# Kernel optimization log

Measured on AMD Instinct MI355X. Metric: run time of the kernel, lower is better.

The kernel has to match this reference:

```python
import jax, jax.numpy as jnp
import numpy as np

N_BITS = 32
HIDDEN = 128


def _neighborhoods(z):
    """z: (B,k,H,W) -> (B,k,9,H,W) 3x3 neighborhoods (zero-padded), center zeroed.

    Position ordering matches F.unfold(kernel_size=3): row-major over (di,dj),
    so index 4 is the center, which the module masks to 0.
    """
    B, k, H, W = z.shape
    zp = jnp.pad(z, ((0, 0), (0, 0), (1, 1), (1, 1)))
    views = []
    for di in range(3):
        for dj in range(3):
            if di == 1 and dj == 1:  # center masked out
                views.append(jnp.zeros_like(z))
            else:
                views.append(zp[:, :, di:di + H, dj:dj + W])
    return jnp.stack(views, axis=2)  # (B,k,9,H,W)


def setup_inputs() -> dict:
    key = jax.random.key(0)
    k1, k2, k3, k4, k5 = jax.random.split(key, 5)
    B, k, H, W = 8, N_BITS, 256, 256
    z = jax.random.normal(k1, (B, k, H, W), dtype=jnp.float32)
    # nn.Linear(9*k, hidden): weight (hidden, 9k), feature order = k-outer, 9-inner
    W1 = jax.random.normal(k2, (HIDDEN, 9 * k), dtype=jnp.float32) * (1.0 / np.sqrt(9 * k))
    b1 = jax.random.normal(k3, (HIDDEN,), dtype=jnp.float32) * 0.01
    W2 = jax.random.normal(k4, (k, HIDDEN), dtype=jnp.float32) * (1.0 / np.sqrt(HIDDEN))
    b2 = jax.random.normal(k5, (k,), dtype=jnp.float32) * 0.01
    return {"z": z, "W1": W1, "b1": b1, "W2": W2, "b2": b2}


def reference(z, W1, b1, W2, b2):
    B, k, H, W = z.shape
    win = _neighborhoods(z)                      # (B,k,9,H,W)
    W1r = W1.reshape(HIDDEN, k, 9)               # split (9k) -> (k,9), k-outer
    h = jnp.einsum('bkphw,dkp->bdhw', win, W1r) + b1[None, :, None, None]
    h = jax.nn.relu(h)
    logits = jnp.einsum('bdhw,kd->bkhw', h, W2) + b2[None, :, None, None]
    return logits  # (B,k,H,W)
```

## Files before the change

kernel.cpp:

```cpp
#include <hip/hip_runtime.h>


#define KC 32
#define HH 256
#define WW 256
#define HID 128
#define YS 8
#define ZROW 2640

typedef __attribute__((ext_vector_type(8))) short short8;
typedef __attribute__((ext_vector_type(4))) float f32x4;

#define BARRIER() asm volatile("s_waitcnt lgkmcnt(0)\n\ts_barrier" ::: "memory")
#define SCHED_FENCE() asm volatile("" ::: "memory")

__device__ __forceinline__ unsigned short f2bf(float f) {
    union { float f; unsigned int i; } x; x.f = f;
    unsigned int r = x.i + 0x7FFFu + ((x.i >> 16) & 1u);
    return (unsigned short)(r >> 16);
}

__device__ __forceinline__ short8 pack8(const float* v) {
    union { short8 s; unsigned int u[4]; } w;
    union { float f; unsigned int i; } uu[8];
#pragma unroll
    for (int j = 0; j < 8; ++j) uu[j].f = v[j];
#pragma unroll
    for (int k = 0; k < 4; ++k)
        w.u[k] = __builtin_amdgcn_perm(uu[2 * k + 1].i, uu[2 * k].i, 0x07060302u);
    return w.s;
}

__global__ void prep_weights(const float* __restrict__ w1,
                             const float* __restrict__ w2,
                             unsigned short* __restrict__ w1t,
                             unsigned short* __restrict__ w2t) {
    int i = blockIdx.x * 256 + threadIdx.x;
    if (i < 9 * HID * KC) {
        int c = i & 31;
        int d = (i >> 5) & 127;
        int p = i >> 12;
        w1t[i] = f2bf(w1[d * (9 * KC) + c * 9 + p]);
    } else if (i < 9 * HID * KC + KC * HID) {
        int j = i - 9 * HID * KC;
        w2t[j] = f2bf(w2[j]);
    }
}

__global__ __launch_bounds__(256, 3) void local_pred_kernel(
    const float* __restrict__ zg,
    const unsigned short* __restrict__ w1t,
    const float* __restrict__ b1g,
    const unsigned short* __restrict__ w2t,
    const float* __restrict__ b2g,
    float* __restrict__ outg)
{
    __shared__ __attribute__((aligned(16))) unsigned short z_lds[4 * ZROW];
    __shared__ __attribute__((aligned(16))) unsigned short h_lds[64 * 136];
    __shared__ __attribute__((aligned(16))) unsigned short halo_lds[7 * 2 * 32];

    const int tid  = threadIdx.x;
    const int bidx = blockIdx.x;
    const int x0 = (bidx & 3) << 6;
    const int y0 = ((bidx >> 2) & 31) * YS;
    const int b  = bidx >> 7;

    const int l = tid & 63;
    const int o = tid >> 6;

    const int wave = tid >> 6;
    const int lane = tid & 63;
    const int lr = lane & 15;
    const int lq = lane >> 4;

    const float* zb = zg + (size_t)b * KC * HH * WW;

#pragma unroll
    for (int dy = 0; dy < 3; ++dy) {
        const int gy = y0 - 1 + dy;
        const bool ok = (unsigned)gy < (unsigned)HH;
        const int gyc = ok ? gy : 0;
        const float* p = zb + ((size_t)(o * 8) * HH + gyc) * WW + x0 + l;
        float t8[8];
#pragma unroll
        for (int j = 0; j < 8; ++j) t8[j] = ok ? p[(size_t)j * HH * WW] : 0.f;
        *(short8*)&z_lds[(dy * 66 + l + 1) * 40 + o * 8] = pack8(t8);
        SCHED_FENCE();
    }
    {
        const int s = tid & 1, oc = (tid >> 1) & 3, dy = tid >> 3;
        const int gy = y0 - 1 + dy;
        const int gx = x0 - 1 + s * 65;
        const bool ok = (tid < 24) && ((unsigned)gy < (unsigned)HH) &&
                        ((unsigned)gx < (unsigned)WW);
        const float* q = zb + ((size_t)(oc * 8) * HH + (ok ? gy : 0)) * WW + (ok ? gx : 0);
        float t8[8];
#pragma unroll
        for (int j = 0; j < 8; ++j) t8[j] = ok ? q[(size_t)j * HH * WW] : 0.f;
        if (tid < 24)
            *(short8*)&z_lds[(dy * 66 + s * 65) * 40 + oc * 8] = pack8(t8);
        SCHED_FENCE();
    }
    {
        const int fi = tid - 64;
        const int s = fi & 1, oc = (fi >> 1) & 3, fr = fi >> 3;
        const int gy = y0 + 2 + fr;
        const int gx = x0 - 1 + s * 65;
        const bool ok = (tid >= 64) && (tid < 120) && (gy < HH) &&
                        ((unsigned)gx < (unsigned)WW);
        const float* q = zb + ((size_t)(oc * 8) * HH + (ok ? gy : 0)) * WW + (ok ? gx : 0);
        float t8[8];
#pragma unroll
        for (int j = 0; j < 8; ++j) t8[j] = ok ? q[(size_t)j * HH * WW] : 0.f;
        if (tid >= 64 && tid < 120)
            *(short8*)&halo_lds[(fr * 2 + s) * 32 + oc * 8] = pack8(t8);
        SCHED_FENCE();
    }

    float bias1[2], bias2[2];
#pragma unroll
    for (int nt = 0; nt < 2; ++nt) bias1[nt] = b1g[wave * 32 + nt * 16 + lr];
#pragma unroll
    for (int nt = 0; nt < 2; ++nt) bias2[nt] = b2g[nt * 16 + lr];

    BARRIER();

    const int tap_di[8] = {0, 0, 0, 1, 1, 2, 2, 2};
    const int tap_dj[8] = {0, 1, 2, 0, 2, 0, 1, 2};

    float mv8[8];

#pragma unroll
    for (int r = 0; r < YS; ++r) {
        const int y = y0 + r;
        const int S0 = r & 3, S1 = (r + 1) & 3, S2 = (r + 2) & 3, S3 = (r + 3) & 3;

        if (r < 7) {
            const int gy = y + 2;
            const bool ok = gy < HH;
            const float* p = zb + ((size_t)(o * 8) * HH + (ok ? gy : 0)) * WW + x0 + l;
#pragma unroll
            for (int j = 0; j < 8; ++j) mv8[j] = ok ? p[(size_t)j * HH * WW] : 0.f;
        }
        SCHED_FENCE();

        f32x4 acc[4][2];
#pragma unroll
        for (int mt = 0; mt < 4; ++mt)
#pragma unroll
            for (int nt = 0; nt < 2; ++nt)
                acc[mt][nt] = (f32x4){0.f, 0.f, 0.f, 0.f};

        const int rowoff[3] = {S0 * ZROW, S1 * ZROW, S2 * ZROW};
#pragma unroll
        for (int t = 0; t < 8; ++t) {
            const int di = tap_di[t], dj = tap_dj[t];
            const int p = di * 3 + dj;
            short8 afr[4];
#pragma unroll
            for (int mt = 0; mt < 4; ++mt)
                afr[mt] = *(const short8*)&z_lds[rowoff[di] + (mt * 16 + lr + dj) * 40 + lq * 8];
            short8 bfr[2];
#pragma unroll
            for (int nt = 0; nt < 2; ++nt)
                bfr[nt] = *(const short8*)&w1t[p * (HID * KC) + (wave * 32 + nt * 16 + lr) * KC + lq * 8];
#pragma unroll
            for (int nt = 0; nt < 2; ++nt)
#pragma unroll
                for (int mt = 0; mt < 4; ++mt)
                    acc[mt][nt] = __builtin_amdgcn_mfma_f32_16x16x32_bf16(
                        afr[mt], bfr[nt], acc[mt][nt], 0, 0, 0);
        }

#pragma unroll
        for (int nt = 0; nt < 2; ++nt) {
            const int d = wave * 32 + nt * 16 + lr;
#pragma unroll
            for (int mt = 0; mt < 4; ++mt)
#pragma unroll
                for (int rr = 0; rr < 4; ++rr) {
                    float v = acc[mt][nt][rr] + bias1[nt];
                    v = v > 0.f ? v : 0.f;
                    const int m = mt * 16 + lq * 4 + rr;
                    h_lds[m * 136 + d] = f2bf(v);
                }
        }
        BARRIER();

        f32x4 acc2[2];
        acc2[0] = (f32x4){0.f, 0.f, 0.f, 0.f};
        acc2[1] = (f32x4){0.f, 0.f, 0.f, 0.f};
        const int m2 = wave * 16 + lr;
#pragma unroll
        for (int k4 = 0; k4 < 4; ++k4) {
            short8 afr = *(const short8*)&h_lds[m2 * 136 + k4 * 32 + lq * 8];
#pragma unroll
            for (int nt = 0; nt < 2; ++nt) {
                short8 bfr = *(const short8*)&w2t[(nt * 16 + lr) * HID + k4 * 32 + lq * 8];
                acc2[nt] = __builtin_amdgcn_mfma_f32_16x16x32_bf16(afr, bfr, acc2[nt], 0, 0, 0);
            }
        }

#pragma unroll
        for (int nt = 0; nt < 2; ++nt) {
            const int kout = nt * 16 + lr;
            f32x4 pk;
#pragma unroll
            for (int rr = 0; rr < 4; ++rr) pk[rr] = acc2[nt][rr] + bias2[nt];
            const int mb = wave * 16 + lq * 4;
            const size_t off = ((size_t)(b * KC + kout) * HH + y) * WW + x0 + mb;
            *(f32x4*)&outg[off] = pk;
        }

        if (r < 7) {
            *(short8*)&z_lds[(S3 * 66 + l + 1) * 40 + o * 8] = pack8(mv8);
            if (tid < 8) {
                const int side = tid & 1, oct = tid >> 1;
                short8 hv = *(const short8*)&halo_lds[(r * 2 + side) * 32 + oct * 8];
                *(short8*)&z_lds[(S3 * 66 + side * 65) * 40 + oct * 8] = hv;
            }
        }
        BARRIER();
    }
}

extern "C" void kernel_launch(void* const* d_in, const int* in_sizes, int n_in,
                              void* d_out, int out_size, void* d_ws, size_t ws_size,
                              hipStream_t stream)
{
    const float* z  = (const float*)d_in[0];
    const float* W1 = (const float*)d_in[1];
    const float* b1 = (const float*)d_in[2];
    const float* W2 = (const float*)d_in[3];
    const float* b2 = (const float*)d_in[4];
    float* out = (float*)d_out;
    unsigned short* w1t = (unsigned short*)d_ws;
    unsigned short* w2t = (unsigned short*)d_ws + 9 * HID * KC;

    hipLaunchKernelGGL(prep_weights, dim3(160), dim3(256), 0, stream, W1, W2, w1t, w2t);
    hipLaunchKernelGGL(local_pred_kernel, dim3(8 * 4 * (HH / YS)), dim3(256), 0, stream,
                       z, w1t, b1, w2t, b2, out);
}
```

Before: 174.9 us.

## Preload W1 fragments into registers, transpose MFMA operands, swizzle z LDS layout

W1 bf16 fragments for all 8 taps are loaded into registers once per block, so the per-row global loads inside the tap loop go away. The MFMA operands are swapped so the result is transposed, which lets the bias/ReLU epilogue write four packed bf16 values per store to h_lds instead of scalar stores. The z LDS rows get a padded swizzle (x*40 + (x&~7)) meant to reduce bank conflicts. Launch bounds are relaxed to allow 3-4 waves per EU, and the extra register pressure from holding the fragments may hurt occupancy or cause spills.

```diff
diff --git a/kernel.cpp b/kernel.cpp
--- a/kernel.cpp
+++ b/kernel.cpp
@@ -6,13 +6,16 @@
 #define WW 256
 #define HID 128
 #define YS 8
-#define ZROW 2640
+#define ZSLOT 2696
 
 typedef __attribute__((ext_vector_type(8))) short short8;
+typedef __attribute__((ext_vector_type(4))) short short4v;
 typedef __attribute__((ext_vector_type(4))) float f32x4;
 
 #define BARRIER() asm volatile("s_waitcnt lgkmcnt(0)\n\ts_barrier" ::: "memory")
 #define SCHED_FENCE() asm volatile("" ::: "memory")
+
+__device__ __forceinline__ int zsw(int x) { return x * 40 + (x & ~7); }
 
 __device__ __forceinline__ unsigned short f2bf(float f) {
     union { float f; unsigned int i; } x; x.f = f;
@@ -47,7 +50,8 @@
     }
 }
 
-__global__ __launch_bounds__(256, 3) void local_pred_kernel(
+__global__ __attribute__((amdgpu_flat_work_group_size(256, 256), amdgpu_waves_per_eu(3, 4)))
+void local_pred_kernel(
     const float* __restrict__ zg,
     const unsigned short* __restrict__ w1t,
     const float* __restrict__ b1g,
@@ -55,7 +59,7 @@
     const float* __restrict__ b2g,
     float* __restrict__ outg)
 {
-    __shared__ __attribute__((aligned(16))) unsigned short z_lds[4 * ZROW];
+    __shared__ __attribute__((aligned(16))) unsigned short z_lds[4 * ZSLOT];
     __shared__ __attribute__((aligned(16))) unsigned short h_lds[64 * 136];
     __shared__ __attribute__((aligned(16))) unsigned short halo_lds[7 * 2 * 32];
 
@@ -79,12 +83,11 @@
     for (int dy = 0; dy < 3; ++dy) {
         const int gy = y0 - 1 + dy;
         const bool ok = (unsigned)gy < (unsigned)HH;
-        const int gyc = ok ? gy : 0;
-        const float* p = zb + ((size_t)(o * 8) * HH + gyc) * WW + x0 + l;
+        const float* p = zb + ((size_t)(o * 8) * HH + (ok ? gy : 0)) * WW + x0 + l;
         float t8[8];
 #pragma unroll
         for (int j = 0; j < 8; ++j) t8[j] = ok ? p[(size_t)j * HH * WW] : 0.f;
-        *(short8*)&z_lds[(dy * 66 + l + 1) * 40 + o * 8] = pack8(t8);
+        *(short8*)&z_lds[dy * ZSLOT + zsw(l + 1) + o * 8] = pack8(t8);
         SCHED_FENCE();
     }
     {
@@ -98,7 +101,7 @@
 #pragma unroll
         for (int j = 0; j < 8; ++j) t8[j] = ok ? q[(size_t)j * HH * WW] : 0.f;
         if (tid < 24)
-            *(short8*)&z_lds[(dy * 66 + s * 65) * 40 + oc * 8] = pack8(t8);
+            *(short8*)&z_lds[dy * ZSLOT + zsw(s * 65) + oc * 8] = pack8(t8);
         SCHED_FENCE();
     }
     {
@@ -117,9 +120,21 @@
         SCHED_FENCE();
     }
 
-    float bias1[2], bias2[2];
-#pragma unroll
-    for (int nt = 0; nt < 2; ++nt) bias1[nt] = b1g[wave * 32 + nt * 16 + lr];
+    short8 w1f[8][2];
+    {
+        const int tap_p[8] = {0, 1, 2, 3, 5, 6, 7, 8};
+#pragma unroll
+        for (int t = 0; t < 8; ++t)
+#pragma unroll
+            for (int dt = 0; dt < 2; ++dt)
+                w1f[t][dt] = *(const short8*)
+                    &w1t[tap_p[t] * (HID * KC) + (wave * 32 + dt * 16 + lr) * KC + lq * 8];
+    }
+    f32x4 bias1v[2];
+#pragma unroll
+    for (int dt = 0; dt < 2; ++dt)
+        bias1v[dt] = *(const f32x4*)&b1g[wave * 32 + dt * 16 + lq * 4];
+    float bias2[2];
 #pragma unroll
     for (int nt = 0; nt < 2; ++nt) bias2[nt] = b2g[nt * 16 + lr];
 
@@ -144,46 +159,48 @@
         }
         SCHED_FENCE();
 
-        f32x4 acc[4][2];
-#pragma unroll
-        for (int mt = 0; mt < 4; ++mt)
-#pragma unroll
-            for (int nt = 0; nt < 2; ++nt)
-                acc[mt][nt] = (f32x4){0.f, 0.f, 0.f, 0.f};
-
-        const int rowoff[3] = {S0 * ZROW, S1 * ZROW, S2 * ZROW};
+        f32x4 accT[2][4];
+#pragma unroll
+        for (int dt = 0; dt < 2; ++dt)
+#pragma unroll
+            for (int mt = 0; mt < 4; ++mt)
+                accT[dt][mt] = (f32x4){0.f, 0.f, 0.f, 0.f};
+
+        const int rowoff[3] = {S0 * ZSLOT, S1 * ZSLOT, S2 * ZSLOT};
 #pragma unroll
         for (int t = 0; t < 8; ++t) {
             const int di = tap_di[t], dj = tap_dj[t];
-            const int p = di * 3 + dj;
-            short8 afr[4];
+            short8 bfr[4];
 #pragma unroll
             for (int mt = 0; mt < 4; ++mt)
-                afr[mt] = *(const short8*)&z_lds[rowoff[di] + (mt * 16 + lr + dj) * 40 + lq * 8];
-            short8 bfr[2];
-#pragma unroll
-            for (int nt = 0; nt < 2; ++nt)
-                bfr[nt] = *(const short8*)&w1t[p * (HID * KC) + (wave * 32 + nt * 16 + lr) * KC + lq * 8];
-#pragma unroll
-            for (int nt = 0; nt < 2; ++nt)
+                bfr[mt] = *(const short8*)&z_lds[rowoff[di] + zsw(mt * 16 + lr + dj) + lq * 8];
+#pragma unroll
+            for (int dt = 0; dt < 2; ++dt)
 #pragma unroll
                 for (int mt = 0; mt < 4; ++mt)
-                    acc[mt][nt] = __builtin_amdgcn_mfma_f32_16x16x32_bf16(
-                        afr[mt], bfr[nt], acc[mt][nt], 0, 0, 0);
-        }
-
-#pragma unroll
-        for (int nt = 0; nt < 2; ++nt) {
-            const int d = wave * 32 + nt * 16 + lr;
-#pragma unroll
-            for (int mt = 0; mt < 4; ++mt)
-#pragma unroll
-                for (int rr = 0; rr < 4; ++rr) {
-                    float v = acc[mt][nt][rr] + bias1[nt];
-                    v = v > 0.f ? v : 0.f;
-                    const int m = mt * 16 + lq * 4 + rr;
-                    h_lds[m * 136 + d] = f2bf(v);
+                    accT[dt][mt] = __builtin_amdgcn_mfma_f32_16x16x32_bf16(
+                        w1f[t][dt], bfr[mt], accT[dt][mt], 0, 0, 0);
+        }
+
+#pragma unroll
+        for (int dt = 0; dt < 2; ++dt) {
+#pragma unroll
+            for (int mt = 0; mt < 4; ++mt) {
+                unsigned int lo, hi;
+                {
+                    float v0 = accT[dt][mt][0] + bias1v[dt][0]; v0 = v0 > 0.f ? v0 : 0.f;
+                    float v1 = accT[dt][mt][1] + bias1v[dt][1]; v1 = v1 > 0.f ? v1 : 0.f;
+                    float v2 = accT[dt][mt][2] + bias1v[dt][2]; v2 = v2 > 0.f ? v2 : 0.f;
+                    float v3 = accT[dt][mt][3] + bias1v[dt][3]; v3 = v3 > 0.f ? v3 : 0.f;
+                    lo = (unsigned int)f2bf(v0) | ((unsigned int)f2bf(v1) << 16);
+                    hi = (unsigned int)f2bf(v2) | ((unsigned int)f2bf(v3) << 16);
                 }
+                union { short4v s; unsigned int u[2]; } pk;
+                pk.u[0] = lo; pk.u[1] = hi;
+                const int m = mt * 16 + lr;
+                const int d = wave * 32 + dt * 16 + lq * 4;
+                *(short4v*)&h_lds[m * 136 + d] = pk.s;
+            }
         }
         BARRIER();
 
@@ -213,11 +230,11 @@
         }
 
         if (r < 7) {
-            *(short8*)&z_lds[(S3 * 66 + l + 1) * 40 + o * 8] = pack8(mv8);
+            *(short8*)&z_lds[S3 * ZSLOT + zsw(l + 1) + o * 8] = pack8(mv8);
             if (tid < 8) {
                 const int side = tid & 1, oct = tid >> 1;
                 short8 hv = *(const short8*)&halo_lds[(r * 2 + side) * 32 + oct * 8];
-                *(short8*)&z_lds[(S3 * 66 + side * 65) * 40 + oct * 8] = hv;
+                *(short8*)&z_lds[S3 * ZSLOT + zsw(side * 65) + oct * 8] = hv;
             }
         }
         BARRIER();
```

Result: slower. 198.1 us (+13.2%).
